# Kernel tuning notes

Hardware: AMD Instinct MI355X
Metric: run time of the kernel (lower is better)

The kernel has to match this reference:

```python
import jax, jax.numpy as jnp
import numpy as np

B, N, D, DFF, E, K, H = 8, 1024, 512, 2048, 8, 2, 8


def setup_inputs() -> dict:
    key = jax.random.key(0)
    ks = jax.random.split(key, 20)
    p = lambda k, shape: (jax.random.normal(k, shape, jnp.float32) * 0.02)
    x = jax.random.normal(ks[0], (B, N, D), jnp.float32)
    adj = (jax.random.uniform(ks[1], (B, N, N)) > 0.5).astype(jnp.float32)
    return {
        "x": x,
        "adj": adj,
        "gc_w": p(ks[2], (D, D)),
        "gc_b": jnp.zeros((D,), jnp.float32),
        "root_emb": p(ks[3], (1, D)),
        "in_w": p(ks[4], (3 * D, D)),
        "in_b": jnp.zeros((3 * D,), jnp.float32),
        "out_w": p(ks[5], (D, D)),
        "out_b": jnp.zeros((D,), jnp.float32),
        "ln1_g": jnp.ones((D,), jnp.float32),
        "ln1_b": jnp.zeros((D,), jnp.float32),
        "ln2_g": jnp.ones((D,), jnp.float32),
        "ln2_b": jnp.zeros((D,), jnp.float32),
        "gate_w": p(ks[6], (E, D)),
        "W1": p(ks[7], (E, D, DFF)),
        "b1": jnp.zeros((E, DFF), jnp.float32),
        "W2": p(ks[8], (E, DFF, D)),
        "b2": jnp.zeros((E, D), jnp.float32),
    }


def layer_norm(x, g, b, eps=1e-5):
    mu = jnp.mean(x, axis=-1, keepdims=True)
    var = jnp.var(x, axis=-1, keepdims=True)
    return (x - mu) * jax.lax.rsqrt(var + eps) * g + b


def reference(x, adj, gc_w, gc_b, root_emb, in_w, in_b, out_w, out_b,
              ln1_g, ln1_b, ln2_g, ln2_b, gate_w, W1, b1, W2, b2):
    b, n, d = x.shape
    h = H
    hd = d // h
    # GraphConv: adj @ x -> linear -> + root embedding (index 0 for every batch)
    g = jnp.einsum('bij,bjd->bid', adj, x) @ gc_w.T + gc_b + root_emb[0]
    x = x + g
    # MultiheadAttention (self-attn, eval mode, no mask)
    qkv = x @ in_w.T + in_b                      # [B,N,3D]
    q, k, v = jnp.split(qkv, 3, axis=-1)
    to_heads = lambda t: t.reshape(b, n, h, hd).transpose(0, 2, 1, 3)
    q, k, v = to_heads(q), to_heads(k), to_heads(v)
    scale = jnp.float32(1.0) / jnp.sqrt(jnp.float32(hd))
    scores = jnp.einsum('bhqe,bhke->bhqk', q * scale, k)
    attn = jax.nn.softmax(scores, axis=-1)
    o = jnp.einsum('bhqk,bhke->bhqe', attn, v).transpose(0, 2, 1, 3).reshape(b, n, d)
    o = o @ out_w.T + out_b
    x = layer_norm(x + o, ln1_g, ln1_b)
    # MoE: top-k gating, normalized weights, weighted sum of expert FFN outputs
    xf = x.reshape(-1, d)                        # [T,D]
    t = xf.shape[0]
    gate_probs = jax.nn.softmax(xf @ gate_w.T, axis=-1)        # [T,E]
    topk_p, topk_i = jax.lax.top_k(gate_probs, K)
    topk_p = topk_p / jnp.sum(topk_p, axis=-1, keepdims=True)
    num_e = gate_w.shape[0]
    w = jnp.zeros((t, num_e), xf.dtype).at[jnp.arange(t)[:, None], topk_i].add(topk_p)
    hid = jax.nn.gelu(jnp.einsum('td,edf->etf', xf, W1) + b1[:, None, :], approximate=False)
    y = jnp.einsum('etf,efd->etd', hid, W2) + b2[:, None, :]   # [E,T,D]
    moe = jnp.einsum('te,etd->td', w, y).reshape(b, n, d)
    return layer_norm(x + moe, ln2_g, ln2_b)
```

## Files before the change

kernel.cpp:

```cpp
#include <hip/hip_runtime.h>
#include <hip/hip_bf16.h>

#define NB 8
#define NSEQ 1024
#define DMODEL 512
#define DF 2048
#define NEXP 8
#define NHEAD 8
#define HDIM 64
#define T_TOK (NB * NSEQ)

typedef unsigned short u16;
typedef float f32x4_t __attribute__((ext_vector_type(4)));
typedef __bf16 bf16x8_t __attribute__((ext_vector_type(8)));

__device__ __forceinline__ u16 f2b(float f) {
  __hip_bfloat16 h = __float2bfloat16(f);
  return *reinterpret_cast<u16*>(&h);
}
__device__ __forceinline__ float b2f(u16 u) {
  return __uint_as_float((unsigned)u << 16);
}
__device__ __forceinline__ void gl_lds16(const u16* g, u16* l) {
  __builtin_amdgcn_global_load_lds(
      (const __attribute__((address_space(1))) unsigned int*)g,
      (__attribute__((address_space(3))) unsigned int*)l, 16, 0, 0);
}

__global__ __launch_bounds__(256) void k_cvt_hl(const float* __restrict__ src,
                                                u16* __restrict__ hi,
                                                u16* __restrict__ lo, int n4) {
  const int i = blockIdx.x * 256 + threadIdx.x;
  if (i >= n4) return;
  const float4 v = ((const float4*)src)[i];
  ushort4 h, l;
  h.x = f2b(v.x); l.x = f2b(v.x - b2f(h.x));
  h.y = f2b(v.y); l.y = f2b(v.y - b2f(h.y));
  h.z = f2b(v.z); l.z = f2b(v.z - b2f(h.z));
  h.w = f2b(v.w); l.w = f2b(v.w - b2f(h.w));
  ((ushort4*)hi)[i] = h;
  ((ushort4*)lo)[i] = l;
}

__global__ __launch_bounds__(256) void k_cvt_b(const float* __restrict__ src,
                                               u16* __restrict__ dst, int n4) {
  const int i = blockIdx.x * 256 + threadIdx.x;
  if (i >= n4) return;
  const float4 v = ((const float4*)src)[i];
  ushort4 h;
  h.x = f2b(v.x); h.y = f2b(v.y); h.z = f2b(v.z); h.w = f2b(v.w);
  ((ushort4*)dst)[i] = h;
}

__global__ __launch_bounds__(256) void k_cvt_t_hl(const float* __restrict__ src,
                                                  u16* __restrict__ hi,
                                                  u16* __restrict__ lo,
                                                  int R, int C) {
  const int z = blockIdx.z;
  src += (size_t)z * R * C;
  hi += (size_t)z * R * C;
  lo += (size_t)z * R * C;
  const int r0 = blockIdx.y * 64, c0 = blockIdx.x * 64;
  __shared__ u16 th[64][65], tl[64][65];
  const int t = threadIdx.x;
  const int cc = t & 63, rb = t >> 6;
#pragma unroll
  for (int i = 0; i < 16; ++i) {
    const int r = i * 4 + rb;
    const float f = src[(size_t)(r0 + r) * C + c0 + cc];
    const u16 h = f2b(f);
    th[r][cc] = h;
    tl[r][cc] = f2b(f - b2f(h));
  }
  __syncthreads();
#pragma unroll
  for (int i = 0; i < 16; ++i) {
    const int r = i * 4 + rb;
    hi[(size_t)(c0 + r) * R + r0 + cc] = th[cc][r];
    lo[(size_t)(c0 + r) * R + r0 + cc] = tl[cc][r];
  }
}

template <int TERMS, int EP>
__global__ __launch_bounds__(256) void k_gemm_sp(
    const u16* __restrict__ Ah, const u16* __restrict__ Al,
    const u16* __restrict__ Bh, const u16* __restrict__ Bl,
    const float* __restrict__ bias, const float* __restrict__ addv,
    const float* __restrict__ addm, float* __restrict__ outF,
    u16* __restrict__ outH, u16* __restrict__ outL,
    u16* __restrict__ outVH, u16* __restrict__ outVL, int K, int N,
    size_t aStride, size_t bStride, size_t cStride) {
  const int z = blockIdx.z;
  Ah += (size_t)z * aStride;
  if (TERMS == 3) Al += (size_t)z * aStride;
  Bh += (size_t)z * bStride;
  Bl += (size_t)z * bStride;
  const int m0 = blockIdx.y * 128, n0 = blockIdx.x * 128;
  __shared__ u16 Ash[128][64];
  __shared__ u16 Asl[(TERMS == 3) ? 128 : 1][64];
  __shared__ u16 Bsh[128][64];
  __shared__ u16 Bsl[128][64];
  const int t = threadIdx.x;
  const int w = t >> 6, l = t & 63;
  const int srow = w * 8 + (l >> 3);
  const int sscol = ((l & 7) ^ (l >> 3)) * 8;
  size_t aoff[4], boff[4];
#pragma unroll
  for (int i = 0; i < 4; ++i) {
    aoff[i] = (size_t)(m0 + i * 32 + srow) * K + sscol;
    boff[i] = (size_t)(n0 + i * 32 + srow) * K + sscol;
  }
  const int wr = w >> 1, wc = w & 1;
  const int lr = l & 15, lg = l >> 4;
  f32x4_t acc[4][4] = {};
  for (int k0 = 0; k0 < K; k0 += 64) {
#pragma unroll
    for (int i = 0; i < 4; ++i) {
      gl_lds16(Ah + aoff[i] + k0, &Ash[i * 32 + w * 8][0]);
      if (TERMS == 3) gl_lds16(Al + aoff[i] + k0, &Asl[i * 32 + w * 8][0]);
      gl_lds16(Bh + boff[i] + k0, &Bsh[i * 32 + w * 8][0]);
      gl_lds16(Bl + boff[i] + k0, &Bsl[i * 32 + w * 8][0]);
    }
    __syncthreads();
#pragma unroll
    for (int kk = 0; kk < 2; ++kk) {
      const int cs = (kk * 32 + lg * 8) ^ ((lr & 7) << 3);
      bf16x8_t ah[4], al[4], bh[4], bl[4];
#pragma unroll
      for (int m = 0; m < 4; ++m) {
        ah[m] = *(const bf16x8_t*)&Ash[wr * 64 + m * 16 + lr][cs];
        if (TERMS == 3)
          al[m] = *(const bf16x8_t*)&Asl[wr * 64 + m * 16 + lr][cs];
      }
#pragma unroll
      for (int n = 0; n < 4; ++n) {
        bh[n] = *(const bf16x8_t*)&Bsh[wc * 64 + n * 16 + lr][cs];
        bl[n] = *(const bf16x8_t*)&Bsl[wc * 64 + n * 16 + lr][cs];
      }
#pragma unroll
      for (int m = 0; m < 4; ++m)
#pragma unroll
        for (int n = 0; n < 4; ++n) {
          acc[m][n] = __builtin_amdgcn_mfma_f32_16x16x32_bf16(ah[m], bh[n],
                                                              acc[m][n], 0, 0, 0);
          acc[m][n] = __builtin_amdgcn_mfma_f32_16x16x32_bf16(ah[m], bl[n],
                                                              acc[m][n], 0, 0, 0);
          if (TERMS == 3)
            acc[m][n] = __builtin_amdgcn_mfma_f32_16x16x32_bf16(
                al[m], bh[n], acc[m][n], 0, 0, 0);
        }
    }
    __syncthreads();
  }
  const size_t cb = (size_t)z * cStride;
#pragma unroll
  for (int m = 0; m < 4; ++m) {
#pragma unroll
    for (int n = 0; n < 4; ++n) {
      const int c = n0 + wc * 64 + n * 16 + lr;
#pragma unroll
      for (int j = 0; j < 4; ++j) {
        const int r = m0 + wr * 64 + m * 16 + lg * 4 + j;
        float v = acc[m][n][j];
        if (EP == 1) v += bias[c] + addv[c] + addm[(size_t)r * N + c];
        if (EP == 2 || EP == 4) v += bias[c];
        const size_t idx = cb + (size_t)r * N + c;
        if (EP == 1 || EP == 2) outF[idx] = v;
        if (EP == 0 || EP == 1) {
          const u16 h = f2b(v);
          outH[idx] = h;
          outL[idx] = f2b(v - b2f(h));
        }
        if (EP == 4) {
          if (c < DMODEL) v *= 0.125f;
          const u16 h = f2b(v);
          const u16 lo = f2b(v - b2f(h));
          if (c < 2 * DMODEL) {
            outH[idx] = h;
            outL[idx] = lo;
          } else {
            const int d = (c - 2 * DMODEL) & 63;
            const int hd = (c - 2 * DMODEL) >> 6;
            const int bb = r >> 10;
            const int tile = (r & 1023) >> 6;
            const int tv = r & 63;
            const int cc2 = 4 * (tv & 15) + (tv >> 4);
            const int stc = cc2 ^ ((d & 7) << 3);
            const size_t vo =
                (((size_t)(bb * 8 + hd) * 16 + tile) * 64 + d) * 64 + stc;
            outVH[vo] = h;
            outVL[vo] = lo;
          }
        }
      }
    }
  }
}

__global__ __launch_bounds__(256) void k_attn(const u16* __restrict__ qh_g,
                                              const u16* __restrict__ ql_g,
                                              const u16* __restrict__ vph,
                                              const u16* __restrict__ vpl,
                                              u16* __restrict__ oh_g,
                                              u16* __restrict__ ol_g) {
  const int q0 = blockIdx.x * 64, h = blockIdx.y, b = blockIdx.z;
  const int t = threadIdx.x;
  const int w = t >> 6, l = t & 63;
  const int lr = l & 15, lg = l >> 4;
  __shared__ u16 Ksh[64][64], Ksl[64][64];
  __shared__ u16 Vth[64][64], Vtl[64][64];
  __shared__ u16 Psh[64][64], Psl[64][64];
  u16* VthF = &Vth[0][0];
  u16* VtlF = &Vtl[0][0];
  bf16x8_t qh[2], ql[2];
  {
    const size_t qoff =
        (size_t)(b * NSEQ + q0 + w * 16 + lr) * (3 * DMODEL) + h * HDIM;
#pragma unroll
    for (int kc = 0; kc < 2; ++kc) {
      qh[kc] = *(const bf16x8_t*)(qh_g + qoff + kc * 32 + lg * 8);
      ql[kc] = *(const bf16x8_t*)(ql_g + qoff + kc * 32 + lg * 8);
    }
  }
  float mrow[4] = {-1e30f, -1e30f, -1e30f, -1e30f};
  float lrow[4] = {0.f, 0.f, 0.f, 0.f};
  f32x4_t acc_o[4] = {};
  const int sr = t >> 2;
  const int sc = (t & 3) * 16;
  const size_t vbh = ((size_t)(b * 8 + h) * 16) * 4096;
  const int vsub = w * 512 + l * 8;
  for (int k0 = 0; k0 < NSEQ; k0 += 64) {
    __syncthreads();
    {
      const size_t kro =
          (size_t)(b * NSEQ + k0 + sr) * (3 * DMODEL) + DMODEL + h * HDIM + sc;
      const uint4 kh0 = *(const uint4*)(qh_g + kro);
      const uint4 kh1 = *(const uint4*)(qh_g + kro + 8);
      const uint4 kl0 = *(const uint4*)(ql_g + kro);
      const uint4 kl1 = *(const uint4*)(ql_g + kro + 8);
      const int cs0 = sc ^ ((sr & 7) << 3);
      const int cs1 = (sc + 8) ^ ((sr & 7) << 3);
      *(uint4*)&Ksh[sr][cs0] = kh0;
      *(uint4*)&Ksh[sr][cs1] = kh1;
      *(uint4*)&Ksl[sr][cs0] = kl0;
      *(uint4*)&Ksl[sr][cs1] = kl1;
      const size_t vt = vbh + (size_t)(k0 >> 6) * 4096;
      gl_lds16(vph + vt + vsub, VthF + w * 512);
      gl_lds16(vph + vt + 2048 + vsub, VthF + 2048 + w * 512);
      gl_lds16(vpl + vt + vsub, VtlF + w * 512);
      gl_lds16(vpl + vt + 2048 + vsub, VtlF + 2048 + w * 512);
    }
    __syncthreads();
    f32x4_t sacc[4] = {};
#pragma unroll
    for (int kc = 0; kc < 2; ++kc) {
#pragma unroll
      for (int n = 0; n < 4; ++n) {
        const int cs = (kc * 32 + lg * 8) ^ ((lr & 7) << 3);
        const bf16x8_t kh = *(const bf16x8_t*)&Ksh[n * 16 + lr][cs];
        const bf16x8_t kl = *(const bf16x8_t*)&Ksl[n * 16 + lr][cs];
        sacc[n] = __builtin_amdgcn_mfma_f32_16x16x32_bf16(qh[kc], kh, sacc[n], 0, 0, 0);
        sacc[n] = __builtin_amdgcn_mfma_f32_16x16x32_bf16(qh[kc], kl, sacc[n], 0, 0, 0);
        sacc[n] = __builtin_amdgcn_mfma_f32_16x16x32_bf16(ql[kc], kh, sacc[n], 0, 0, 0);
      }
    }
    float alpha[4];
#pragma unroll
    for (int j = 0; j < 4; ++j) {
      float mx = fmaxf(fmaxf(sacc[0][j], sacc[1][j]),
                       fmaxf(sacc[2][j], sacc[3][j]));
      mx = fmaxf(mx, __shfl_xor(mx, 1));
      mx = fmaxf(mx, __shfl_xor(mx, 2));
      mx = fmaxf(mx, __shfl_xor(mx, 4));
      mx = fmaxf(mx, __shfl_xor(mx, 8));
      const float mnew = fmaxf(mrow[j], mx);
      alpha[j] = __expf(mrow[j] - mnew);
      mrow[j] = mnew;
      float psum = 0.f;
      const int prow = lg * 4 + j;
      ushort4 ph4, pl4;
      u16* php = (u16*)&ph4;
      u16* plp = (u16*)&pl4;
#pragma unroll
      for (int n = 0; n < 4; ++n) {
        const float p = __expf(sacc[n][j] - mnew);
        psum += p;
        const u16 hi = f2b(p);
        php[n] = hi;
        plp[n] = f2b(p - b2f(hi));
      }
      const int pc = (4 * lr) ^ ((prow & 7) << 3);
      *(ushort4*)&Psh[w * 16 + prow][pc] = ph4;
      *(ushort4*)&Psl[w * 16 + prow][pc] = pl4;
      psum += __shfl_xor(psum, 1);
      psum += __shfl_xor(psum, 2);
      psum += __shfl_xor(psum, 4);
      psum += __shfl_xor(psum, 8);
      lrow[j] = lrow[j] * alpha[j] + psum;
    }
#pragma unroll
    for (int n = 0; n < 4; ++n) {
#pragma unroll
      for (int j = 0; j < 4; ++j) acc_o[n][j] *= alpha[j];
    }
#pragma unroll
    for (int kc = 0; kc < 2; ++kc) {
      const int cs = (kc * 32 + lg * 8) ^ ((lr & 7) << 3);
      const bf16x8_t ph = *(const bf16x8_t*)&Psh[w * 16 + lr][cs];
      const bf16x8_t pl = *(const bf16x8_t*)&Psl[w * 16 + lr][cs];
#pragma unroll
      for (int n = 0; n < 4; ++n) {
        const bf16x8_t vh = *(const bf16x8_t*)&Vth[n * 16 + lr][cs];
        const bf16x8_t vl = *(const bf16x8_t*)&Vtl[n * 16 + lr][cs];
        acc_o[n] = __builtin_amdgcn_mfma_f32_16x16x32_bf16(ph, vh, acc_o[n], 0, 0, 0);
        acc_o[n] = __builtin_amdgcn_mfma_f32_16x16x32_bf16(ph, vl, acc_o[n], 0, 0, 0);
        acc_o[n] = __builtin_amdgcn_mfma_f32_16x16x32_bf16(pl, vh, acc_o[n], 0, 0, 0);
      }
    }
  }
#pragma unroll
  for (int j = 0; j < 4; ++j) {
    const float invl = 1.0f / lrow[j];
    const size_t ro =
        (size_t)(b * NSEQ + q0 + w * 16 + lg * 4 + j) * DMODEL + h * HDIM;
#pragma unroll
    for (int n = 0; n < 4; ++n) {
      const float v = acc_o[n][j] * invl;
      const u16 hh = f2b(v);
      oh_g[ro + n * 16 + lr] = hh;
      ol_g[ro + n * 16 + lr] = f2b(v - b2f(hh));
    }
  }
}

__global__ __launch_bounds__(256) void k_ln_add(
    const float* __restrict__ a, const float* __restrict__ bsrc,
    const float* __restrict__ g, const float* __restrict__ be,
    float* __restrict__ outp, u16* __restrict__ outb) {
  const int tok = blockIdx.x;
  const int t = threadIdx.x;
  float2 v;
  {
    const float2 va = *(const float2*)(a + (size_t)tok * DMODEL + t * 2);
    const float2 vb = *(const float2*)(bsrc + (size_t)tok * DMODEL + t * 2);
    v.x = va.x + vb.x; v.y = va.y + vb.y;
  }
  float s1 = v.x + v.y, s2 = v.x * v.x + v.y * v.y;
#pragma unroll
  for (int o = 32; o; o >>= 1) { s1 += __shfl_down(s1, o); s2 += __shfl_down(s2, o); }
  __shared__ float sm1[4], sm2[4];
  if ((t & 63) == 0) { sm1[t >> 6] = s1; sm2[t >> 6] = s2; }
  __syncthreads();
  s1 = sm1[0] + sm1[1] + sm1[2] + sm1[3];
  s2 = sm2[0] + sm2[1] + sm2[2] + sm2[3];
  const float mean = s1 * (1.f / DMODEL);
  const float var = s2 * (1.f / DMODEL) - mean * mean;
  const float rstd = rsqrtf(var + 1e-5f);
  float2 o;
  o.x = (v.x - mean) * rstd * g[t * 2] + be[t * 2];
  o.y = (v.y - mean) * rstd * g[t * 2 + 1] + be[t * 2 + 1];
  *(float2*)(outp + (size_t)tok * DMODEL + t * 2) = o;
  ushort2 ob;
  ob.x = f2b(o.x); ob.y = f2b(o.y);
  *(ushort2*)(outb + (size_t)tok * DMODEL + t * 2) = ob;
}

__global__ __launch_bounds__(256) void k_gate(const float* __restrict__ x2,
                                              const float* __restrict__ gw,
                                              int* __restrict__ eidx,
                                              float* __restrict__ ewgt) {
  const int t = threadIdx.x;
  const int g = t >> 4;
  const int s = t & 15;
  const int tok = blockIdx.x * 16 + g;
  float acc[NEXP] = {};
  const float* px = x2 + (size_t)tok * DMODEL + s * 32;
  const float* pw = gw + s * 32;
#pragma unroll
  for (int i = 0; i < 32; i += 4) {
    const float4 xv = *(const float4*)(px + i);
#pragma unroll
    for (int e = 0; e < NEXP; ++e) {
      const float4 wv = *(const float4*)(pw + e * DMODEL + i);
      acc[e] += xv.x * wv.x + xv.y * wv.y + xv.z * wv.z + xv.w * wv.w;
    }
  }
#pragma unroll
  for (int e = 0; e < NEXP; ++e) {
    acc[e] += __shfl_xor(acc[e], 1);
    acc[e] += __shfl_xor(acc[e], 2);
    acc[e] += __shfl_xor(acc[e], 4);
    acc[e] += __shfl_xor(acc[e], 8);
  }
  if (s == 0) {
    int i0 = 0; float b0 = acc[0];
#pragma unroll
    for (int e = 1; e < NEXP; ++e) if (acc[e] > b0) { b0 = acc[e]; i0 = e; }
    int i1 = -1; float v1 = -1e30f;
#pragma unroll
    for (int e = 0; e < NEXP; ++e)
      if (e != i0 && acc[e] > v1) { v1 = acc[e]; i1 = e; }
    const float tt = __expf(v1 - b0);
    const float w0 = 1.f / (1.f + tt), w1 = tt / (1.f + tt);
    eidx[tok * 2] = i0; eidx[tok * 2 + 1] = i1;
    ewgt[tok * 2] = w0; ewgt[tok * 2 + 1] = w1;
  }
}

__global__ void k_zero(int* __restrict__ p, int n) {
  const int i = blockIdx.x * blockDim.x + threadIdx.x;
  if (i < n) p[i] = 0;
}

__global__ __launch_bounds__(256) void k_count(const int* __restrict__ eidx,
                                               int* __restrict__ ecnt) {
  __shared__ int cnt[NEXP];
  const int t = threadIdx.x;
  if (t < NEXP) cnt[t] = 0;
  __syncthreads();
  atomicAdd(&cnt[eidx[blockIdx.x * 256 + t]], 1);
  __syncthreads();
  if (t < NEXP) atomicAdd(&ecnt[t], cnt[t]);
}

__global__ void k_offsets(const int* __restrict__ ecnt, int* __restrict__ eoff) {
  if (threadIdx.x == 0) {
    int s = 0;
    for (int e = 0; e < NEXP; ++e) { eoff[e] = s; s += ecnt[e]; }
  }
}

__global__ __launch_bounds__(256) void k_scatter(
    const int* __restrict__ eidx, const int* __restrict__ eoff,
    int* __restrict__ efill, int* __restrict__ rtok, int* __restrict__ t2s) {
  __shared__ int lcnt[NEXP];
  __shared__ int lbase[NEXP];
  const int t = threadIdx.x;
  if (t < NEXP) lcnt[t] = 0;
  __syncthreads();
  const int tok = blockIdx.x * 128 + (t >> 1);
  const int k = t & 1;
  const int e = eidx[tok * 2 + k];
  const int lpos = atomicAdd(&lcnt[e], 1);
  __syncthreads();
  if (t < NEXP) lbase[t] = atomicAdd(&efill[t], lcnt[t]);
  __syncthreads();
  const int slot = eoff[e] + lbase[e] + lpos;
  rtok[slot] = tok;
  t2s[tok * 2 + k] = slot;
}

__global__ __launch_bounds__(256) void k_cvt_t(const float* __restrict__ src,
                                               u16* __restrict__ dst,
                                               int R, int C) {
  const int e = blockIdx.z;
  src += (size_t)e * R * C;
  dst += (size_t)e * R * C;
  const int r0 = blockIdx.y * 64, c0 = blockIdx.x * 64;
  __shared__ u16 tile[64][65];
  const int t = threadIdx.x;
  const int cc = t & 63, rb = t >> 6;
#pragma unroll
  for (int i = 0; i < 16; ++i) {
    const int r = i * 4 + rb;
    tile[r][cc] = f2b(src[(size_t)(r0 + r) * C + c0 + cc]);
  }
  __syncthreads();
#pragma unroll
  for (int i = 0; i < 16; ++i) {
    const int r = i * 4 + rb;
    dst[(size_t)(c0 + r) * R + r0 + cc] = tile[cc][r];
  }
}

template <int MODE>
__global__ __launch_bounds__(256) void k_moe_mfma(
    const u16* __restrict__ Ab, const u16* __restrict__ Bb,
    const float* __restrict__ bias, const int* __restrict__ rtok,
    const int* __restrict__ ecnt, const int* __restrict__ eoff,
    u16* __restrict__ outp) {
  constexpr int K = (MODE == 0) ? DMODEL : DF;
  constexpr int N = (MODE == 0) ? DF : DMODEL;
  const int e = blockIdx.z;
  const int cnt = ecnt[e];
  const int m0 = blockIdx.y * 128;
  if (m0 >= cnt) return;
  const int off = eoff[e];
  const int n0 = blockIdx.x * 128;
  const u16* Bw = Bb + (size_t)e * (size_t)K * N;
  __shared__ u16 As[128][64];
  __shared__ u16 Bs[128][64];
  const int t = threadIdx.x;
  const int w = t >> 6, l = t & 63;
  const int srow = w * 8 + (l >> 3);
  const int sscol = ((l & 7) ^ (l >> 3)) * 8;
  const u16* arow[4];
#pragma unroll
  for (int i = 0; i < 4; ++i) {
    const int r = m0 + i * 32 + srow;
    const int rr = (r < cnt) ? r : (cnt - 1);
    if (MODE == 0)
      arow[i] = Ab + (size_t)rtok[off + rr] * K + sscol;
    else
      arow[i] = Ab + ((size_t)off + rr) * K + sscol;
  }
  const u16* brow[4];
#pragma unroll
  for (int i = 0; i < 4; ++i)
    brow[i] = Bw + (size_t)(n0 + i * 32 + srow) * K + sscol;

  const int wr = w >> 1, wc = w & 1;
  const int lr = l & 15, lg = l >> 4;
  f32x4_t acc[4][4] = {};
  for (int k0 = 0; k0 < K; k0 += 64) {
#pragma unroll
    for (int i = 0; i < 4; ++i) {
      gl_lds16(arow[i] + k0, &As[i * 32 + w * 8][0]);
      gl_lds16(brow[i] + k0, &Bs[i * 32 + w * 8][0]);
    }
    __syncthreads();
#pragma unroll
    for (int kk = 0; kk < 2; ++kk) {
      const int cs = (kk * 32 + lg * 8) ^ ((lr & 7) << 3);
      bf16x8_t af[4], bfr[4];
#pragma unroll
      for (int m = 0; m < 4; ++m)
        af[m] = *(const bf16x8_t*)&As[wr * 64 + m * 16 + lr][cs];
#pragma unroll
      for (int n = 0; n < 4; ++n)
        bfr[n] = *(const bf16x8_t*)&Bs[wc * 64 + n * 16 + lr][cs];
#pragma unroll
      for (int m = 0; m < 4; ++m)
#pragma unroll
        for (int n = 0; n < 4; ++n)
          acc[m][n] = __builtin_amdgcn_mfma_f32_16x16x32_bf16(
              af[m], bfr[n], acc[m][n], 0, 0, 0);
    }
    __syncthreads();
  }
#pragma unroll
  for (int m = 0; m < 4; ++m) {
    const int rl0 = wr * 64 + m * 16 + lg * 4;
#pragma unroll
    for (int n = 0; n < 4; ++n) {
      const int gc = n0 + wc * 64 + n * 16 + lr;
      const float bv = bias[e * N + gc];
#pragma unroll
      for (int j = 0; j < 4; ++j) {
        const int r = m0 + rl0 + j;
        if (r < cnt) {
          float v = acc[m][n][j] + bv;
          if (MODE == 0) v = v * 0.5f * (1.f + erff(v * 0.70710678118f));
          outp[((size_t)off + r) * N + gc] = f2b(v);
        }
      }
    }
  }
}

__global__ __launch_bounds__(256) void k_ln2(
    const float* __restrict__ x2, const u16* __restrict__ ybuf,
    const int* __restrict__ t2s, const float* __restrict__ ewgt,
    const float* __restrict__ g, const float* __restrict__ be,
    float* __restrict__ outp) {
  const int tok = blockIdx.x;
  const int t = threadIdx.x;
  const int s0 = t2s[tok * 2], s1i = t2s[tok * 2 + 1];
  const float w0 = ewgt[tok * 2], w1 = ewgt[tok * 2 + 1];
  float2 v;
  {
    const float2 a = *(const float2*)(x2 + (size_t)tok * DMODEL + t * 2);
    const ushort2 y0 = *(const ushort2*)(ybuf + (size_t)s0 * DMODEL + t * 2);
    const ushort2 y1 = *(const ushort2*)(ybuf + (size_t)s1i * DMODEL + t * 2);
    v.x = a.x + w0 * b2f(y0.x) + w1 * b2f(y1.x);
    v.y = a.y + w0 * b2f(y0.y) + w1 * b2f(y1.y);
  }
  float sum1 = v.x + v.y, sum2 = v.x * v.x + v.y * v.y;
#pragma unroll
  for (int o = 32; o; o >>= 1) { sum1 += __shfl_down(sum1, o); sum2 += __shfl_down(sum2, o); }
  __shared__ float sm1[4], sm2[4];
  if ((t & 63) == 0) { sm1[t >> 6] = sum1; sm2[t >> 6] = sum2; }
  __syncthreads();
  sum1 = sm1[0] + sm1[1] + sm1[2] + sm1[3];
  sum2 = sm2[0] + sm2[1] + sm2[2] + sm2[3];
  const float mean = sum1 * (1.f / DMODEL);
  const float var = sum2 * (1.f / DMODEL) - mean * mean;
  const float rstd = rsqrtf(var + 1e-5f);
  float2 o;
  o.x = (v.x - mean) * rstd * g[t * 2] + be[t * 2];
  o.y = (v.y - mean) * rstd * g[t * 2 + 1] + be[t * 2 + 1];
  *(float2*)(outp + (size_t)tok * DMODEL + t * 2) = o;
}

extern "C" void kernel_launch(void* const* d_in, const int* in_sizes, int n_in,
                              void* d_out, int out_size, void* d_ws,
                              size_t ws_size, hipStream_t stream) {
  const float* x      = (const float*)d_in[0];
  const float* adj    = (const float*)d_in[1];
  const float* gc_w   = (const float*)d_in[2];
  const float* gc_b   = (const float*)d_in[3];
  const float* root   = (const float*)d_in[4];
  const float* in_w   = (const float*)d_in[5];
  const float* in_b   = (const float*)d_in[6];
  const float* out_w  = (const float*)d_in[7];
  const float* out_b  = (const float*)d_in[8];
  const float* ln1_g  = (const float*)d_in[9];
  const float* ln1_b  = (const float*)d_in[10];
  const float* ln2_g  = (const float*)d_in[11];
  const float* ln2_b  = (const float*)d_in[12];
  const float* gate_w = (const float*)d_in[13];
  const float* W1     = (const float*)d_in[14];
  const float* b1     = (const float*)d_in[15];
  const float* W2     = (const float*)d_in[16];
  const float* b2     = (const float*)d_in[17];
  float* outp = (float*)d_out;

  constexpr size_t MB = 1ull << 20;
  char* W = (char*)d_ws;
  u16*   adj_bf = (u16*)(W + 0);
  u16*   xht    = (u16*)(W + 16 * MB);
  u16*   xlt    = (u16*)(W + 24 * MB);
  u16*   axh    = (u16*)(W + 32 * MB);
  u16*   axl    = (u16*)(W + 40 * MB);
  float* x1     = (float*)(W + 48 * MB);
  u16*   x1h    = (u16*)(W + 64 * MB);
  u16*   x1l    = (u16*)(W + 72 * MB);
  u16*   qkvh   = (u16*)(W + 0);
  u16*   qkvl   = (u16*)(W + 24 * MB);
  u16*   vph    = (u16*)(W + 80 * MB);
  u16*   vpl    = (u16*)(W + 88 * MB);
  u16*   oatth  = (u16*)(W + 96 * MB);
  u16*   oattl  = (u16*)(W + 104 * MB);
  float* oproj  = (float*)(W + 0);
  float* x2     = (float*)(W + 96 * MB);
  u16*   Wxb    = (u16*)(W + 80 * MB);
  u16*   hid    = (u16*)(W + 16 * MB);
  u16*   ybuf   = (u16*)(W + 0);
  char*  misc   = W + 112 * MB;
  char*  Od     = (char*)d_out;
  u16*   gwh = (u16*)(Od + 0);
  u16*   gwl = (u16*)(Od + 512 * 1024);
  u16*   iwh = (u16*)(Od + 1 * MB);
  u16*   iwl = (u16*)(Od + 1 * MB + 1536 * 1024);
  u16*   owh = (u16*)(Od + 4 * MB);
  u16*   owl = (u16*)(Od + 4 * MB + 512 * 1024);
  u16*   x2b = (u16*)d_out;
  int*   eidx  = (int*)misc;
  float* ewgt  = (float*)(misc + 65536);
  int*   ecnt  = (int*)(misc + 131072);
  int*   eoff  = (int*)(misc + 131072 + 128);
  int*   efill = (int*)(misc + 131072 + 256);
  int*   rtok  = (int*)(misc + 131072 + 512);
  int*   t2s   = (int*)(misc + 131072 + 512 + 65536);

  k_cvt_b<<<dim3(8192), 256, 0, stream>>>(adj, adj_bf, NB * NSEQ * NSEQ / 4);
  k_cvt_t_hl<<<dim3(8, 16, 8), 256, 0, stream>>>(x, xht, xlt, NSEQ, DMODEL);
  k_cvt_hl<<<dim3(256), 256, 0, stream>>>(gc_w, gwh, gwl, DMODEL * DMODEL / 4);
  k_cvt_hl<<<dim3(768), 256, 0, stream>>>(in_w, iwh, iwl, 3 * DMODEL * DMODEL / 4);
  k_cvt_hl<<<dim3(256), 256, 0, stream>>>(out_w, owh, owl, DMODEL * DMODEL / 4);
  k_gemm_sp<2, 0><<<dim3(4, 8, 8), 256, 0, stream>>>(
      adj_bf, nullptr, xht, xlt, nullptr, nullptr, nullptr, nullptr, axh, axl,
      nullptr, nullptr, NSEQ, DMODEL, (size_t)NSEQ * NSEQ,
      (size_t)DMODEL * NSEQ, (size_t)NSEQ * DMODEL);
  k_gemm_sp<3, 1><<<dim3(4, 64, 1), 256, 0, stream>>>(
      axh, axl, gwh, gwl, gc_b, root, x, x1, x1h, x1l, nullptr, nullptr,
      DMODEL, DMODEL, 0, 0, 0);
  k_gemm_sp<3, 4><<<dim3(12, 64, 1), 256, 0, stream>>>(
      x1h, x1l, iwh, iwl, in_b, nullptr, nullptr, nullptr, qkvh, qkvl, vph,
      vpl, DMODEL, 3 * DMODEL, 0, 0, 0);
  k_attn<<<dim3(16, 8, 8), 256, 0, stream>>>(qkvh, qkvl, vph, vpl, oatth,
                                             oattl);
  k_gemm_sp<3, 2><<<dim3(4, 64, 1), 256, 0, stream>>>(
      oatth, oattl, owh, owl, out_b, nullptr, nullptr, oproj, nullptr, nullptr,
      nullptr, nullptr, DMODEL, DMODEL, 0, 0, 0);
  k_ln_add<<<dim3(T_TOK), 256, 0, stream>>>(x1, oproj, ln1_g, ln1_b, x2, x2b);
  k_zero<<<dim3(1), 128, 0, stream>>>((int*)(misc + 131072), 128);
  k_gate<<<dim3(T_TOK / 16), 256, 0, stream>>>(x2, gate_w, eidx, ewgt);
  k_count<<<dim3(2 * T_TOK / 256), 256, 0, stream>>>(eidx, ecnt);
  k_offsets<<<dim3(1), 64, 0, stream>>>(ecnt, eoff);
  k_scatter<<<dim3(T_TOK / 128), 256, 0, stream>>>(eidx, eoff, efill, rtok,
                                                   t2s);
  k_cvt_t<<<dim3(DF / 64, DMODEL / 64, NEXP), 256, 0, stream>>>(W1, Wxb,
                                                                DMODEL, DF);
  k_moe_mfma<0><<<dim3(DF / 128, 128, NEXP), 256, 0, stream>>>(
      x2b, Wxb, b1, rtok, ecnt, eoff, hid);
  k_cvt_t<<<dim3(DMODEL / 64, DF / 64, NEXP), 256, 0, stream>>>(W2, Wxb, DF,
                                                                DMODEL);
  k_moe_mfma<1><<<dim3(DMODEL / 128, 128, NEXP), 256, 0, stream>>>(
      hid, Wxb, b2, rtok, ecnt, eoff, ybuf);
  k_ln2<<<dim3(T_TOK), 256, 0, stream>>>(x2, ybuf, t2s, ewgt, ln2_g, ln2_b,
                                         outp);
}
```

Before: 518.7 us.

## Double query tile per attention block and register-prefetch next K/V tile

The attention kernel now handles 128 query rows per block (two 64-row sub-tiles per wave), so each K/V tile loaded into shared memory is reused twice and the grid is halved. The next K/V tile is prefetched into registers while the current tile is computed, replacing the synchronous loads and global-to-LDS copies. s_setprio hints are placed around the MFMA sections. This raises register pressure and doubles the P staging buffer in LDS, which may reduce occupancy, and with the smaller grid there are fewer blocks to spread across the CUs.

```diff
diff --git a/kernel.cpp b/kernel.cpp
--- a/kernel.cpp
+++ b/kernel.cpp
@@ -203,132 +203,180 @@
                                               const u16* __restrict__ vpl,
                                               u16* __restrict__ oh_g,
                                               u16* __restrict__ ol_g) {
-  const int q0 = blockIdx.x * 64, h = blockIdx.y, b = blockIdx.z;
+  const int q0 = blockIdx.x * 128, h = blockIdx.y, b = blockIdx.z;
   const int t = threadIdx.x;
   const int w = t >> 6, l = t & 63;
   const int lr = l & 15, lg = l >> 4;
   __shared__ u16 Ksh[64][64], Ksl[64][64];
   __shared__ u16 Vth[64][64], Vtl[64][64];
-  __shared__ u16 Psh[64][64], Psl[64][64];
+  __shared__ u16 Psh[128][64], Psl[128][64];
   u16* VthF = &Vth[0][0];
   u16* VtlF = &Vtl[0][0];
-  bf16x8_t qh[2], ql[2];
-  {
+  bf16x8_t qh[2][2], ql[2][2];
+#pragma unroll
+  for (int s = 0; s < 2; ++s) {
     const size_t qoff =
-        (size_t)(b * NSEQ + q0 + w * 16 + lr) * (3 * DMODEL) + h * HDIM;
+        (size_t)(b * NSEQ + q0 + s * 64 + w * 16 + lr) * (3 * DMODEL) +
+        h * HDIM;
 #pragma unroll
     for (int kc = 0; kc < 2; ++kc) {
-      qh[kc] = *(const bf16x8_t*)(qh_g + qoff + kc * 32 + lg * 8);
-      ql[kc] = *(const bf16x8_t*)(ql_g + qoff + kc * 32 + lg * 8);
-    }
-  }
-  float mrow[4] = {-1e30f, -1e30f, -1e30f, -1e30f};
-  float lrow[4] = {0.f, 0.f, 0.f, 0.f};
-  f32x4_t acc_o[4] = {};
+      qh[s][kc] = *(const bf16x8_t*)(qh_g + qoff + kc * 32 + lg * 8);
+      ql[s][kc] = *(const bf16x8_t*)(ql_g + qoff + kc * 32 + lg * 8);
+    }
+  }
+  float mrow[2][4], lrow[2][4];
+#pragma unroll
+  for (int s = 0; s < 2; ++s)
+#pragma unroll
+    for (int j = 0; j < 4; ++j) { mrow[s][j] = -1e30f; lrow[s][j] = 0.f; }
+  f32x4_t acc_o[2][4] = {};
   const int sr = t >> 2;
   const int sc = (t & 3) * 16;
+  const int cs0 = sc ^ ((sr & 7) << 3);
+  const int cs1 = (sc + 8) ^ ((sr & 7) << 3);
   const size_t vbh = ((size_t)(b * 8 + h) * 16) * 4096;
   const int vsub = w * 512 + l * 8;
+  uint4 pkh0, pkh1, pkl0, pkl1, pvh0, pvh1, pvl0, pvl1;
+  {
+    const size_t kro =
+        (size_t)(b * NSEQ + sr) * (3 * DMODEL) + DMODEL + h * HDIM + sc;
+    pkh0 = *(const uint4*)(qh_g + kro);
+    pkh1 = *(const uint4*)(qh_g + kro + 8);
+    pkl0 = *(const uint4*)(ql_g + kro);
+    pkl1 = *(const uint4*)(ql_g + kro + 8);
+    pvh0 = *(const uint4*)(vph + vbh + vsub);
+    pvh1 = *(const uint4*)(vph + vbh + 2048 + vsub);
+    pvl0 = *(const uint4*)(vpl + vbh + vsub);
+    pvl1 = *(const uint4*)(vpl + vbh + 2048 + vsub);
+  }
   for (int k0 = 0; k0 < NSEQ; k0 += 64) {
     __syncthreads();
-    {
-      const size_t kro =
-          (size_t)(b * NSEQ + k0 + sr) * (3 * DMODEL) + DMODEL + h * HDIM + sc;
-      const uint4 kh0 = *(const uint4*)(qh_g + kro);
-      const uint4 kh1 = *(const uint4*)(qh_g + kro + 8);
-      const uint4 kl0 = *(const uint4*)(ql_g + kro);
-      const uint4 kl1 = *(const uint4*)(ql_g + kro + 8);
-      const int cs0 = sc ^ ((sr & 7) << 3);
-      const int cs1 = (sc + 8) ^ ((sr & 7) << 3);
-      *(uint4*)&Ksh[sr][cs0] = kh0;
-      *(uint4*)&Ksh[sr][cs1] = kh1;
-      *(uint4*)&Ksl[sr][cs0] = kl0;
-      *(uint4*)&Ksl[sr][cs1] = kl1;
-      const size_t vt = vbh + (size_t)(k0 >> 6) * 4096;
-      gl_lds16(vph + vt + vsub, VthF + w * 512);
-      gl_lds16(vph + vt + 2048 + vsub, VthF + 2048 + w * 512);
-      gl_lds16(vpl + vt + vsub, VtlF + w * 512);
-      gl_lds16(vpl + vt + 2048 + vsub, VtlF + 2048 + w * 512);
-    }
+    *(uint4*)&Ksh[sr][cs0] = pkh0;
+    *(uint4*)&Ksh[sr][cs1] = pkh1;
+    *(uint4*)&Ksl[sr][cs0] = pkl0;
+    *(uint4*)&Ksl[sr][cs1] = pkl1;
+    *(uint4*)(VthF + vsub) = pvh0;
+    *(uint4*)(VthF + 2048 + vsub) = pvh1;
+    *(uint4*)(VtlF + vsub) = pvl0;
+    *(uint4*)(VtlF + 2048 + vsub) = pvl1;
     __syncthreads();
-    f32x4_t sacc[4] = {};
+    if (k0 + 64 < NSEQ) {
+      const size_t kro = (size_t)(b * NSEQ + k0 + 64 + sr) * (3 * DMODEL) +
+                         DMODEL + h * HDIM + sc;
+      pkh0 = *(const uint4*)(qh_g + kro);
+      pkh1 = *(const uint4*)(qh_g + kro + 8);
+      pkl0 = *(const uint4*)(ql_g + kro);
+      pkl1 = *(const uint4*)(ql_g + kro + 8);
+      const size_t vt = vbh + (size_t)((k0 >> 6) + 1) * 4096;
+      pvh0 = *(const uint4*)(vph + vt + vsub);
+      pvh1 = *(const uint4*)(vph + vt + 2048 + vsub);
+      pvl0 = *(const uint4*)(vpl + vt + vsub);
+      pvl1 = *(const uint4*)(vpl + vt + 2048 + vsub);
+    }
+    f32x4_t sacc[2][4] = {};
+    __builtin_amdgcn_s_setprio(1);
 #pragma unroll
     for (int kc = 0; kc < 2; ++kc) {
+      const int cs = (kc * 32 + lg * 8) ^ ((lr & 7) << 3);
 #pragma unroll
       for (int n = 0; n < 4; ++n) {
-        const int cs = (kc * 32 + lg * 8) ^ ((lr & 7) << 3);
         const bf16x8_t kh = *(const bf16x8_t*)&Ksh[n * 16 + lr][cs];
         const bf16x8_t kl = *(const bf16x8_t*)&Ksl[n * 16 + lr][cs];
-        sacc[n] = __builtin_amdgcn_mfma_f32_16x16x32_bf16(qh[kc], kh, sacc[n], 0, 0, 0);
-        sacc[n] = __builtin_amdgcn_mfma_f32_16x16x32_bf16(qh[kc], kl, sacc[n], 0, 0, 0);
-        sacc[n] = __builtin_amdgcn_mfma_f32_16x16x32_bf16(ql[kc], kh, sacc[n], 0, 0, 0);
-      }
-    }
-    float alpha[4];
-#pragma unroll
-    for (int j = 0; j < 4; ++j) {
-      float mx = fmaxf(fmaxf(sacc[0][j], sacc[1][j]),
-                       fmaxf(sacc[2][j], sacc[3][j]));
-      mx = fmaxf(mx, __shfl_xor(mx, 1));
-      mx = fmaxf(mx, __shfl_xor(mx, 2));
-      mx = fmaxf(mx, __shfl_xor(mx, 4));
-      mx = fmaxf(mx, __shfl_xor(mx, 8));
-      const float mnew = fmaxf(mrow[j], mx);
-      alpha[j] = __expf(mrow[j] - mnew);
-      mrow[j] = mnew;
-      float psum = 0.f;
-      const int prow = lg * 4 + j;
-      ushort4 ph4, pl4;
-      u16* php = (u16*)&ph4;
-      u16* plp = (u16*)&pl4;
-#pragma unroll
-      for (int n = 0; n < 4; ++n) {
-        const float p = __expf(sacc[n][j] - mnew);
-        psum += p;
-        const u16 hi = f2b(p);
-        php[n] = hi;
-        plp[n] = f2b(p - b2f(hi));
-      }
-      const int pc = (4 * lr) ^ ((prow & 7) << 3);
-      *(ushort4*)&Psh[w * 16 + prow][pc] = ph4;
-      *(ushort4*)&Psl[w * 16 + prow][pc] = pl4;
-      psum += __shfl_xor(psum, 1);
-      psum += __shfl_xor(psum, 2);
-      psum += __shfl_xor(psum, 4);
-      psum += __shfl_xor(psum, 8);
-      lrow[j] = lrow[j] * alpha[j] + psum;
-    }
-#pragma unroll
-    for (int n = 0; n < 4; ++n) {
-#pragma unroll
-      for (int j = 0; j < 4; ++j) acc_o[n][j] *= alpha[j];
-    }
+#pragma unroll
+        for (int s = 0; s < 2; ++s) {
+          sacc[s][n] = __builtin_amdgcn_mfma_f32_16x16x32_bf16(
+              qh[s][kc], kh, sacc[s][n], 0, 0, 0);
+          sacc[s][n] = __builtin_amdgcn_mfma_f32_16x16x32_bf16(
+              qh[s][kc], kl, sacc[s][n], 0, 0, 0);
+          sacc[s][n] = __builtin_amdgcn_mfma_f32_16x16x32_bf16(
+              ql[s][kc], kh, sacc[s][n], 0, 0, 0);
+        }
+      }
+    }
+    __builtin_amdgcn_s_setprio(0);
+#pragma unroll
+    for (int s = 0; s < 2; ++s) {
+      float alpha[4];
+#pragma unroll
+      for (int j = 0; j < 4; ++j) {
+        float mx = fmaxf(fmaxf(sacc[s][0][j], sacc[s][1][j]),
+                         fmaxf(sacc[s][2][j], sacc[s][3][j]));
+        mx = fmaxf(mx, __shfl_xor(mx, 1));
+        mx = fmaxf(mx, __shfl_xor(mx, 2));
+        mx = fmaxf(mx, __shfl_xor(mx, 4));
+        mx = fmaxf(mx, __shfl_xor(mx, 8));
+        const float mnew = fmaxf(mrow[s][j], mx);
+        alpha[j] = __expf(mrow[s][j] - mnew);
+        mrow[s][j] = mnew;
+        float psum = 0.f;
+        const int prow = lg * 4 + j;
+        ushort4 ph4, pl4;
+        u16* php = (u16*)&ph4;
+        u16* plp = (u16*)&pl4;
+#pragma unroll
+        for (int n = 0; n < 4; ++n) {
+          const float p = __expf(sacc[s][n][j] - mnew);
+          psum += p;
+          const u16 hi = f2b(p);
+          php[n] = hi;
+          plp[n] = f2b(p - b2f(hi));
+        }
+        const int pc = (4 * lr) ^ ((prow & 7) << 3);
+        *(ushort4*)&Psh[s * 64 + w * 16 + prow][pc] = ph4;
+        *(ushort4*)&Psl[s * 64 + w * 16 + prow][pc] = pl4;
+        psum += __shfl_xor(psum, 1);
+        psum += __shfl_xor(psum, 2);
+        psum += __shfl_xor(psum, 4);
+        psum += __shfl_xor(psum, 8);
+        lrow[s][j] = lrow[s][j] * alpha[j] + psum;
+      }
+#pragma unroll
+      for (int n = 0; n < 4; ++n)
+#pragma unroll
+        for (int j = 0; j < 4; ++j) acc_o[s][n][j] *= alpha[j];
+    }
+    __builtin_amdgcn_s_setprio(1);
 #pragma unroll
     for (int kc = 0; kc < 2; ++kc) {
       const int cs = (kc * 32 + lg * 8) ^ ((lr & 7) << 3);
-      const bf16x8_t ph = *(const bf16x8_t*)&Psh[w * 16 + lr][cs];
-      const bf16x8_t pl = *(const bf16x8_t*)&Psl[w * 16 + lr][cs];
+      bf16x8_t ph[2], pl[2];
+#pragma unroll
+      for (int s = 0; s < 2; ++s) {
+        ph[s] = *(const bf16x8_t*)&Psh[s * 64 + w * 16 + lr][cs];
+        pl[s] = *(const bf16x8_t*)&Psl[s * 64 + w * 16 + lr][cs];
+      }
 #pragma unroll
       for (int n = 0; n < 4; ++n) {
         const bf16x8_t vh = *(const bf16x8_t*)&Vth[n * 16 + lr][cs];
         const bf16x8_t vl = *(const bf16x8_t*)&Vtl[n * 16 + lr][cs];
-        acc_o[n] = __builtin_amdgcn_mfma_f32_16x16x32_bf16(ph, vh, acc_o[n], 0, 0, 0);
-        acc_o[n] = __builtin_amdgcn_mfma_f32_16x16x32_bf16(ph, vl, acc_o[n], 0, 0, 0);
-        acc_o[n] = __builtin_amdgcn_mfma_f32_16x16x32_bf16(pl, vh, acc_o[n], 0, 0, 0);
-      }
-    }
-  }
-#pragma unroll
-  for (int j = 0; j < 4; ++j) {
-    const float invl = 1.0f / lrow[j];
-    const size_t ro =
-        (size_t)(b * NSEQ + q0 + w * 16 + lg * 4 + j) * DMODEL + h * HDIM;
-#pragma unroll
-    for (int n = 0; n < 4; ++n) {
-      const float v = acc_o[n][j] * invl;
-      const u16 hh = f2b(v);
-      oh_g[ro + n * 16 + lr] = hh;
-      ol_g[ro + n * 16 + lr] = f2b(v - b2f(hh));
+#pragma unroll
+        for (int s = 0; s < 2; ++s) {
+          acc_o[s][n] = __builtin_amdgcn_mfma_f32_16x16x32_bf16(
+              ph[s], vh, acc_o[s][n], 0, 0, 0);
+          acc_o[s][n] = __builtin_amdgcn_mfma_f32_16x16x32_bf16(
+              ph[s], vl, acc_o[s][n], 0, 0, 0);
+          acc_o[s][n] = __builtin_amdgcn_mfma_f32_16x16x32_bf16(
+              pl[s], vh, acc_o[s][n], 0, 0, 0);
+        }
+      }
+    }
+    __builtin_amdgcn_s_setprio(0);
+  }
+#pragma unroll
+  for (int s = 0; s < 2; ++s) {
+#pragma unroll
+    for (int j = 0; j < 4; ++j) {
+      const float invl = 1.0f / lrow[s][j];
+      const size_t ro =
+          (size_t)(b * NSEQ + q0 + s * 64 + w * 16 + lg * 4 + j) * DMODEL +
+          h * HDIM;
+#pragma unroll
+      for (int n = 0; n < 4; ++n) {
+        const float v = acc_o[s][n][j] * invl;
+        const u16 hh = f2b(v);
+        oh_g[ro + n * 16 + lr] = hh;
+        ol_g[ro + n * 16 + lr] = f2b(v - b2f(hh));
+      }
     }
   }
 }
@@ -668,8 +716,8 @@
   k_gemm_sp<3, 4><<<dim3(12, 64, 1), 256, 0, stream>>>(
       x1h, x1l, iwh, iwl, in_b, nullptr, nullptr, nullptr, qkvh, qkvl, vph,
       vpl, DMODEL, 3 * DMODEL, 0, 0, 0);
-  k_attn<<<dim3(16, 8, 8), 256, 0, stream>>>(qkvh, qkvl, vph, vpl, oatth,
-                                             oattl);
+  k_attn<<<dim3(8, 8, 8), 256, 0, stream>>>(qkvh, qkvl, vph, vpl, oatth,
+                                            oattl);
   k_gemm_sp<3, 2><<<dim3(4, 64, 1), 256, 0, stream>>>(
       oatth, oattl, owh, owl, out_b, nullptr, nullptr, oproj, nullptr, nullptr,
       nullptr, nullptr, DMODEL, DMODEL, 0, 0, 0);
```

New measurement: 500.0 us. 1.04x faster.
